# Kernel optimization log

Measured on AMD Instinct MI355X. Metric: run time of the kernel, lower is better.

Reference implementation:

```python
import jax, jax.numpy as jnp
import numpy as np
from jax import lax
from jax.scipy.special import logsumexp

GW_WEIGHT = 20.0
GAMMA_P = 0.01
IN_ITER = 5
OUT_ITER = 10
LAMBDA_STEP = 0.01
N1, N2, D = 2048, 2048, 128
EMB_SCALE = 0.05  # keeps exp(-x@x.T) numerically sane, mimics trained embeddings
ADJ_DENSITY = 0.005


def setup_inputs() -> dict:
    key = jax.random.key(0)
    k1, k2, k3, k4 = jax.random.split(key, 4)
    out1 = jax.random.normal(k1, (N1, D), jnp.float32) * EMB_SCALE
    out2 = jax.random.normal(k2, (N2, D), jnp.float32) * EMB_SCALE

    def make_adj(k, n):
        m = (jax.random.uniform(k, (n, n)) < ADJ_DENSITY).astype(jnp.float32)
        m = jnp.maximum(m, m.T)                      # symmetric, like to_dense_adj of undirected graph
        return m * (1.0 - jnp.eye(n, dtype=jnp.float32))

    adj1 = make_adj(k3, N1)
    adj2 = make_adj(k4, N2)
    threshold_lambda = jnp.float32(1.0 / (N1 * N2))  # init_lambda / (n1*n2)
    return {"out1": out1, "out2": out2, "adj1": adj1, "adj2": adj2,
            "threshold_lambda": threshold_lambda}


def sinkhorn_stable(inter_c, intra_c1, intra_c2, gw_weight, gamma_p, lam,
                    in_iter, out_iter):
    """Log-domain (stabilized) entropic GW Sinkhorn.
    Outer loop: linearize the GW cost around current plan s (shifted by lam);
    inner loop: stabilized Sinkhorn with uniform marginals."""
    n1, n2 = inter_c.shape
    dt = inter_c.dtype
    log_mu = jnp.full((n1,), -np.log(n1), dt)
    log_nu = jnp.full((n2,), -np.log(n2), dt)
    c1sq = intra_c1 ** 2
    c2sq = intra_c2 ** 2
    s0 = jnp.full((n1, n2), 1.0 / (n1 * n2), dt)

    def outer_body(_, s):
        s_hat = s - lam
        a = jnp.sum(s_hat, axis=1)                    # [n1]
        b = jnp.sum(s_hat, axis=0)                    # [n2]
        # GW cost linearization: c1^2 a 1^T + 1 b^T c2^2 - 2 c1 s c2^T
        gw_cost = ((c1sq @ a)[:, None] + (b @ c2sq)[None, :]
                   - 2.0 * (intra_c1 @ s_hat @ intra_c2.T))
        cost = inter_c + gw_weight * gw_cost
        K = -cost / gamma_p                           # log kernel

        def inner_body(_, uv):
            u, v = uv
            u = log_mu - logsumexp(K + v[None, :], axis=1)
            v = log_nu - logsumexp(K + u[:, None], axis=0)
            return (u, v)

        u, v = lax.fori_loop(0, in_iter, inner_body,
                             (jnp.zeros((n1,), dt), jnp.zeros((n2,), dt)))
        return jnp.exp(K + u[:, None] + v[None, :])

    return lax.fori_loop(0, out_iter, outer_body, s0)


def _update_lambda(inter_c, intra_c1, intra_c2, s, gw_weight):
    # mid = c1^2 @ 1 * n2 + 1 @ c2^2 * n1 - 2 c1 @ 1 @ c2^T is rank-structured;
    # compute sum(mid*s) and sum(mid) without materializing mid.
    n1, n2 = inter_c.shape
    c1sq = intra_c1 ** 2
    c2sq = intra_c2 ** 2
    r1sq = jnp.sum(c1sq, axis=1)      # rowsum of c1^2  [n1]
    c2s = jnp.sum(c2sq, axis=0)       # colsum of c2^2  [n2]
    rs1 = jnp.sum(intra_c1, axis=1)   # [n1]
    rs2 = jnp.sum(intra_c2, axis=1)   # [n2]
    a_s = jnp.sum(s, axis=1)
    b_s = jnp.sum(s, axis=0)
    k1 = jnp.sum(inter_c)
    k2 = n2 * (r1sq @ a_s) + n1 * (c2s @ b_s) - 2.0 * (rs1 @ (s @ rs2))
    k3 = (n2 * n2) * jnp.sum(r1sq) + (n1 * n1) * jnp.sum(c2s) \
         - 2.0 * jnp.sum(rs1) * jnp.sum(rs2)
    return (k1 + 2.0 * gw_weight * k2) / (2.0 * gw_weight * k3)


def reference(out1, out2, adj1, adj2, threshold_lambda):
    n1, n2 = out1.shape[0], out2.shape[0]
    inter_c = jnp.exp(-(out1 @ out2.T))
    intra_c1 = jnp.exp(-(out1 @ out1.T)) * adj1
    intra_c2 = jnp.exp(-(out2 @ out2.T)) * adj2

    # torch.no_grad() block
    s = sinkhorn_stable(inter_c, intra_c1, intra_c2, GW_WEIGHT, GAMMA_P,
                        threshold_lambda, IN_ITER, OUT_ITER)
    lam = (LAMBDA_STEP * _update_lambda(inter_c, intra_c1, intra_c2, s, GW_WEIGHT)
           + (1.0 - LAMBDA_STEP) * threshold_lambda)

    s_hat = s - lam
    w_loss = jnp.sum(inter_c * s_hat)
    a = jnp.sum(s_hat, axis=1)
    b = jnp.sum(s_hat, axis=0)
    c1sq = intra_c1 ** 2
    c2sq = intra_c2 ** 2
    gw_loss = jnp.sum(((c1sq @ a)[:, None] + (b @ c2sq)[None, :]
                       - 2.0 * (intra_c1 @ s_hat @ intra_c2.T)) * s_hat)
    loss = w_loss + GW_WEIGHT * gw_loss + 20.0
    return (loss, s, lam)
```

## Files before the change

kernel.cpp:

```cpp
#include <hip/hip_runtime.h>
#include <math.h>

#define N 2048
#define DIM 128
#define CAP (N*64)
#define LOGN 7.6246189861593985f

typedef unsigned long long u64;
typedef unsigned int u32;
typedef unsigned short u16;

__device__ __forceinline__ u32 bf16bits(float f) {
  u32 x = __float_as_uint(f);
  return (x + 0x7fffu + ((x >> 16) & 1u)) >> 16;
}
__device__ __forceinline__ u32 pack_bf16x2(float lo, float hi) {
  return bf16bits(lo) | (bf16bits(hi) << 16);
}
__device__ __forceinline__ float bflo(u32 u) { return __uint_as_float(u << 16); }
__device__ __forceinline__ float bfhi(u32 u) { return __uint_as_float(u & 0xffff0000u); }


__global__ __launch_bounds__(256) void k_gemm_inter(
    const float* __restrict__ A, const float* __restrict__ B,
    float* __restrict__ O, double* __restrict__ k1p) {
  __shared__ __align__(16) float As[64][65];
  __shared__ __align__(16) float Bs[64][65];
  __shared__ float red[256];
  const int t = threadIdx.x;
  const int i0 = blockIdx.y * 64, j0 = blockIdx.x * 64;
  const int tx = t & 15, ty = t >> 4;
  float acc[4][4] = {};
  for (int kk = 0; kk < DIM; kk += 64) {
    if (kk) __syncthreads();
    for (int q = t; q < 64 * 16; q += 256) {
      int row = q >> 4, k4 = (q & 15) << 2;
      float4 av = *(const float4*)&A[(size_t)(i0 + row) * DIM + kk + k4];
      As[k4 + 0][row] = av.x; As[k4 + 1][row] = av.y;
      As[k4 + 2][row] = av.z; As[k4 + 3][row] = av.w;
      float4 bv = *(const float4*)&B[(size_t)(j0 + row) * DIM + kk + k4];
      Bs[k4 + 0][row] = bv.x; Bs[k4 + 1][row] = bv.y;
      Bs[k4 + 2][row] = bv.z; Bs[k4 + 3][row] = bv.w;
    }
    __syncthreads();
    #pragma unroll 4
    for (int k = 0; k < 64; ++k) {
      float av[4], bv[4];
      #pragma unroll
      for (int d = 0; d < 4; ++d) { av[d] = As[k][ty * 4 + d]; bv[d] = Bs[k][tx * 4 + d]; }
      #pragma unroll
      for (int di = 0; di < 4; ++di)
        #pragma unroll
        for (int dj = 0; dj < 4; ++dj)
          acc[di][dj] = fmaf(av[di], bv[dj], acc[di][dj]);
    }
  }
  float psum = 0.f;
  #pragma unroll
  for (int di = 0; di < 4; ++di)
    #pragma unroll
    for (int dj = 0; dj < 4; ++dj) {
      float vv = __expf(-acc[di][dj]);
      O[(size_t)(i0 + ty * 4 + di) * N + (j0 + tx * 4 + dj)] = vv;
      psum += vv;
    }
  red[t] = psum; __syncthreads();
  for (int off = 128; off; off >>= 1) { if (t < off) red[t] += red[t + off]; __syncthreads(); }
  if (t == 0) k1p[blockIdx.y * 32 + blockIdx.x] = (double)red[0];
}

__global__ __launch_bounds__(256) void k_count(const float* __restrict__ adj, int* __restrict__ cnt) {
  int i = blockIdx.x * 4 + (threadIdx.x >> 6);
  int lane = threadIdx.x & 63;
  const float* row = adj + (size_t)i * N;
  int c = 0;
  for (int j = lane; j < N; j += 64) c += (row[j] != 0.f) ? 1 : 0;
  for (int off = 32; off; off >>= 1) c += __shfl_down(c, off);
  if (lane == 0) cnt[i] = c;
}

__global__ __launch_bounds__(256) void k_scan(const int* __restrict__ cnt, int* __restrict__ rp) {
  __shared__ int sums[256];
  int t = threadIdx.x;
  int local[8]; int run = 0;
  int base = t * 8;
  #pragma unroll
  for (int k = 0; k < 8; ++k) { local[k] = run; run += cnt[base + k]; }
  sums[t] = run; __syncthreads();
  for (int off = 1; off < 256; off <<= 1) {
    int val = (t >= off) ? sums[t - off] : 0;
    __syncthreads();
    sums[t] += val;
    __syncthreads();
  }
  int pre = (t == 0) ? 0 : sums[t - 1];
  #pragma unroll
  for (int k = 0; k < 8; ++k) rp[base + k] = pre + local[k];
  if (t == 255) rp[N] = sums[255];
}

__global__ __launch_bounds__(256) void k_fill(const float* __restrict__ adj, const int* __restrict__ rp,
                                              int* __restrict__ cols, int* __restrict__ rows) {
  int i = blockIdx.x * 4 + (threadIdx.x >> 6);
  int lane = threadIdx.x & 63;
  const float* row = adj + (size_t)i * N;
  int pos = rp[i];
  for (int j0 = 0; j0 < N; j0 += 64) {
    bool p = row[j0 + lane] != 0.f;
    u64 mask = __ballot(p);
    if (p) {
      int off = __popcll(mask & ((1ull << lane) - 1ull));
      cols[pos + off] = j0 + lane;
      rows[pos + off] = i;
    }
    pos += __popcll(mask);
  }
}

__global__ __launch_bounds__(256) void k_vals(const int* __restrict__ rp, const int* __restrict__ rows,
                                              const int* __restrict__ cols, float* __restrict__ vals,
                                              const float* __restrict__ emb) {
  int lane = threadIdx.x & 63;
  int total = rp[N];
  for (int p = blockIdx.x * 4 + (threadIdx.x >> 6); p < total; p += 8192) {
    int i = rows[p], k = cols[p];
    const float* ei = emb + (size_t)i * DIM;
    const float* ek = emb + (size_t)k * DIM;
    float s = ei[lane] * ek[lane] + ei[lane + 64] * ek[lane + 64];
    for (int off = 32; off; off >>= 1) s += __shfl_down(s, off);
    if (lane == 0) vals[p] = __expf(-s);
  }
}

__global__ __launch_bounds__(256) void k_rowstats(const int* __restrict__ rp, const float* __restrict__ vals,
                                                  float* __restrict__ rs, float* __restrict__ rsq) {
  int i = blockIdx.x * 4 + (threadIdx.x >> 6);
  int lane = threadIdx.x & 63;
  int p0 = rp[i], p1 = rp[i + 1];
  float s1 = 0.f, s2 = 0.f;
  for (int p = p0 + lane; p < p1; p += 64) { float w = vals[p]; s1 += w; s2 += w * w; }
  for (int off = 32; off; off >>= 1) { s1 += __shfl_down(s1, off); s2 += __shfl_down(s2, off); }
  if (lane == 0) { rs[i] = s1; rsq[i] = s2; }
}

template<int V>
__global__ __launch_bounds__(256) void k_spmmt(const int* __restrict__ rp, const int* __restrict__ cols,
                                               const float* __restrict__ vals, const u16* __restrict__ S,
                                               const float* __restrict__ af, const float* __restrict__ bf,
                                               u16* __restrict__ OutB, float* __restrict__ OutF) {
  __shared__ int winc[1024];
  __shared__ float winv[1024];
  __shared__ int rb[9];
  const int t = threadIdx.x;
  const int tile = blockIdx.x & 7;
  const int c = tile * 256 + t;
  const int i0 = (blockIdx.x >> 3) * 8;
  const int p0 = rp[i0];
  if (t < 9) rb[t] = rp[i0 + t] - p0;
  __syncthreads();
  const int nn = rb[8];
  for (int k = t; k < nn; k += 256) {
    int col = cols[p0 + k];
    winc[k] = col << 11;
    winv[k] = (V == 0) ? vals[p0 + k] * af[col] : vals[p0 + k];
  }
  __syncthreads();
  float a[8];
  #pragma unroll
  for (int r = 0; r < 8; ++r) {
    int pe = rb[r + 1];
    int p = rb[r];
    float a0 = 0.f, a1 = 0.f, a2 = 0.f, a3 = 0.f;
    for (; p + 3 < pe; p += 4) {
      a0 = fmaf(winv[p],     __uint_as_float((u32)S[winc[p]     + c] << 16), a0);
      a1 = fmaf(winv[p + 1], __uint_as_float((u32)S[winc[p + 1] + c] << 16), a1);
      a2 = fmaf(winv[p + 2], __uint_as_float((u32)S[winc[p + 2] + c] << 16), a2);
      a3 = fmaf(winv[p + 3], __uint_as_float((u32)S[winc[p + 3] + c] << 16), a3);
    }
    for (; p < pe; ++p) a0 = fmaf(winv[p], __uint_as_float((u32)S[winc[p] + c] << 16), a0);
    a[r] = (a0 + a1) + (a2 + a3);
  }
  size_t ob = (size_t)(tile * 256 + t) * N + i0;
  if (V == 0) {
    float bc = bf[c];
    #pragma unroll
    for (int r = 0; r < 8; ++r) a[r] *= bc;
    uint4 pk;
    pk.x = pack_bf16x2(a[0], a[1]); pk.y = pack_bf16x2(a[2], a[3]);
    pk.z = pack_bf16x2(a[4], a[5]); pk.w = pack_bf16x2(a[6], a[7]);
    *(uint4*)&OutB[ob] = pk;
  } else {
    *(float4*)&OutF[ob]     = make_float4(a[0], a[1], a[2], a[3]);
    *(float4*)&OutF[ob + 4] = make_float4(a[4], a[5], a[6], a[7]);
  }
}

__global__ __launch_bounds__(256) void k_prep(
    int mode,
    const int* __restrict__ rp1, const int* __restrict__ cols1, const float* __restrict__ vals1,
    const float* __restrict__ r1sq, const float* __restrict__ rs1,
    const float* __restrict__ r2sq, const float* __restrict__ lamp,
    const float* __restrict__ as_,
    float* __restrict__ Ai, float* __restrict__ Bj, float* __restrict__ RLi) {
  int g = blockIdx.x * 256 + threadIdx.x;
  float lam = *lamp;
  float f = 0.00048828125f - lam * 2048.f;
  if (mode == 0) {
    if (g < N) {
      Ai[g] = -2000.f * r1sq[g] * f;
      RLi[g] = 4000.f * rs1[g] * (2.384185791015625e-07f - lam);
    } else {
      int j = g - N;
      Bj[j] = -2000.f * r2sq[j] * f;
    }
  } else if (mode == 1) {
    if (g < N) {
      int p0 = rp1[g], p1 = rp1[g + 1];
      float acc = 0.f;
      for (int p = p0; p < p1; ++p) { float w = vals1[p]; acc = fmaf(w * w, as_[cols1[p]], acc); }
      Ai[g] = -2000.f * (acc - lam * 2048.f * r1sq[g]);
      RLi[g] = -4000.f * lam * rs1[g];
    } else {
      int j = g - N;
      Bj[j] = -2000.f * r2sq[j] * f;
    }
  } else {
    if (g < N) {
      int p0 = rp1[g], p1 = rp1[g + 1];
      float acc = 0.f;
      for (int p = p0; p < p1; ++p) { float w = vals1[p]; acc = fmaf(w * w, as_[cols1[p]], acc); }
      Ai[g] = acc;
    } else {
      int j = g - N;
      Bj[j] = r2sq[j] * 0.00048828125f;
    }
  }
}

template<int MODE>
__global__ __launch_bounds__(256) void k_iter(
    u32* __restrict__ P,
    const float* __restrict__ inter, const float* __restrict__ M,
    const float* __restrict__ Ai, const float* __restrict__ Bj,
    const float* __restrict__ RLi, const float* __restrict__ rs2,
    const float* __restrict__ bvec, float* __restrict__ avec,
    float* __restrict__ part) {
  __shared__ u32 Pl[4 * 1024];
  __shared__ float bl[N];
  __shared__ float a4[4];
  const int t = threadIdx.x;
  const int r0 = blockIdx.x * 4;
  const int w = t >> 6, lane = t & 63;
  const int row = r0 + w;

  if (MODE == 0) {
    #pragma unroll
    for (int q = 0; q < 2; ++q) {
      int j = (q * 256 + t) * 4;
      *(float4*)&bl[j] = *(const float4*)&bvec[j];
    }
    #pragma unroll
    for (int q = 0; q < 4; ++q) {
      int g = (q * 256 + t) * 4;
      *(uint4*)&Pl[g] = *(const uint4*)&P[(size_t)r0 * 1024 + g];
    }
    __syncthreads();
    float y = 0.f;
    const u32* Pr = Pl + w * 1024;
    #pragma unroll
    for (int k = 0; k < 16; ++k) {
      int g = lane + k * 64;
      u32 u = Pr[g];
      y = fmaf(bflo(u), bl[2 * g], y);
      y = fmaf(bfhi(u), bl[2 * g + 1], y);
    }
    for (int off = 32; off; off >>= 1) y += __shfl_xor(y, off);
    if (lane == 0) { float aw = 1.f / (2048.f * y); a4[w] = aw; avec[row] = aw; }
  } else {
    float kv[32];
    float m = -INFINITY;
    const float ai_ = Ai[row], rli = RLi[row];
    const float* ir = inter + (size_t)row * N;
    const float* mr = M + (size_t)row * N;
    #pragma unroll
    for (int q = 0; q < 8; ++q) {
      int j = lane * 4 + q * 256;
      float4 iv = *(const float4*)&ir[j];
      float4 bj = *(const float4*)&Bj[j];
      float4 r2 = *(const float4*)&rs2[j];
      float k0 = fmaf(-100.f, iv.x, ai_ + bj.x + rli * r2.x);
      float k1 = fmaf(-100.f, iv.y, ai_ + bj.y + rli * r2.y);
      float k2 = fmaf(-100.f, iv.z, ai_ + bj.z + rli * r2.z);
      float k3 = fmaf(-100.f, iv.w, ai_ + bj.w + rli * r2.w);
      if (MODE == 1) {
        float4 mv = *(const float4*)&mr[j];
        k0 = fmaf(4000.f, mv.x, k0);
        k1 = fmaf(4000.f, mv.y, k1);
        k2 = fmaf(4000.f, mv.z, k2);
        k3 = fmaf(4000.f, mv.w, k3);
      }
      kv[q * 4 + 0] = k0; kv[q * 4 + 1] = k1; kv[q * 4 + 2] = k2; kv[q * 4 + 3] = k3;
      m = fmaxf(m, fmaxf(fmaxf(k0, k1), fmaxf(k2, k3)));
    }
    for (int off = 32; off; off >>= 1) m = fmaxf(m, __shfl_xor(m, off));
    float ss = 0.f;
    #pragma unroll
    for (int q = 0; q < 8; ++q) {
      float p0 = __expf(kv[q * 4 + 0] - m);
      float p1 = __expf(kv[q * 4 + 1] - m);
      float p2 = __expf(kv[q * 4 + 2] - m);
      float p3 = __expf(kv[q * 4 + 3] - m);
      ss += (p0 + p1) + (p2 + p3);
      u32 lo = pack_bf16x2(p0, p1), hi = pack_bf16x2(p2, p3);
      int g = lane * 2 + q * 128;
      Pl[w * 1024 + g] = lo; Pl[w * 1024 + g + 1] = hi;
      *(uint2*)&P[(size_t)row * 1024 + g] = make_uint2(lo, hi);
    }
    for (int off = 32; off; off >>= 1) ss += __shfl_xor(ss, off);
    if (lane == 0) { float aw = 1.f / (2048.f * ss); a4[w] = aw; avec[row] = aw; }
  }
  __syncthreads();
  const float a0 = a4[0], a1 = a4[1], a2 = a4[2], a3 = a4[3];
  #pragma unroll
  for (int k = 0; k < 4; ++k) {
    int g = k * 256 + t;
    u32 u0 = Pl[g], u1 = Pl[1024 + g], u2 = Pl[2048 + g], u3 = Pl[3072 + g];
    float zlo = bflo(u0) * a0 + bflo(u1) * a1 + bflo(u2) * a2 + bflo(u3) * a3;
    float zhi = bfhi(u0) * a0 + bfhi(u1) * a1 + bfhi(u2) * a2 + bfhi(u3) * a3;
    *(float2*)&part[(size_t)blockIdx.x * N + 2 * g] = make_float2(zlo, zhi);
  }
}

__global__ __launch_bounds__(256) void k_comb(const float* __restrict__ part, float* __restrict__ bvec) {
  __shared__ float pp[16][17];
  const int t = threadIdx.x;
  const int cl = t & 15, kg = t >> 4;
  const int c = blockIdx.x * 16 + cl;
  float z = 0.f;
  for (int k = kg * 32; k < kg * 32 + 32; ++k) z += part[(size_t)k * N + c];
  pp[kg][cl] = z;
  __syncthreads();
  if (t < 16) {
    float zz = 0.f;
    #pragma unroll
    for (int g = 0; g < 16; ++g) zz += pp[g][t];
    bvec[blockIdx.x * 16 + t] = 1.f / (2048.f * zz);
  }
}

__global__ __launch_bounds__(256) void k_rowfin(const u32* __restrict__ P, const float* __restrict__ bvec,
                                                const float* __restrict__ avec, float* __restrict__ as_) {
  __shared__ float bl[N];
  const int t = threadIdx.x;
  #pragma unroll
  for (int q = 0; q < 2; ++q) {
    int j = (q * 256 + t) * 4;
    *(float4*)&bl[j] = *(const float4*)&bvec[j];
  }
  __syncthreads();
  const int w = t >> 6, lane = t & 63;
  const int row = blockIdx.x * 4 + w;
  const u32* Pr = P + (size_t)row * 1024;
  float y = 0.f;
  #pragma unroll
  for (int k = 0; k < 16; ++k) {
    int g = lane + k * 64;
    u32 u = Pr[g];
    y = fmaf(bflo(u), bl[2 * g], y);
    y = fmaf(bfhi(u), bl[2 * g + 1], y);
  }
  for (int off = 32; off; off >>= 1) y += __shfl_xor(y, off);
  if (lane == 0) as_[row] = avec[row] * y;
}

__global__ __launch_bounds__(256) void k_fstats(
    const float* __restrict__ inter, const u32* __restrict__ P, const float* __restrict__ M,
    const float* __restrict__ rs2, const float* __restrict__ avec, const float* __restrict__ bvec,
    float* __restrict__ sOut, float* __restrict__ sisr, float* __restrict__ yv,
    double* __restrict__ dotp) {
  __shared__ __align__(16) float r2[N];
  __shared__ __align__(16) float bl[N];
  __shared__ double redm[4];
  const int t = threadIdx.x;
  #pragma unroll
  for (int q = 0; q < 2; ++q) {
    int j = (q * 256 + t) * 4;
    *(float4*)&r2[j] = *(const float4*)&rs2[j];
    *(float4*)&bl[j] = *(const float4*)&bvec[j];
  }
  __syncthreads();
  const int w = t >> 6, lane = t & 63;
  const int row = blockIdx.x * 4 + w;
  const float av = avec[row];
  const float* ir = inter + (size_t)row * N;
  const float* mr = M + (size_t)row * N;
  const u32* Pr = P + (size_t)row * 1024;
  float* sr = sOut + (size_t)row * N;
  float d1 = 0.f, d2 = 0.f;
  double dm = 0.0;
  #pragma unroll 4
  for (int k = 0; k < 16; ++k) {
    int g = lane + k * 64;
    int j = 2 * g;
    u32 u = Pr[g];
    float s0 = bflo(u) * av * bl[j];
    float s1 = bfhi(u) * av * bl[j + 1];
    float2 iv = *(const float2*)&ir[j];
    float2 mv = *(const float2*)&mr[j];
    sr[j] = s0; sr[j + 1] = s1;
    d1 += iv.x * s0 + iv.y * s1;
    d2 += s0 * r2[j] + s1 * r2[j + 1];
    dm += (double)(mv.x * s0) + (double)(mv.y * s1);
  }
  for (int off = 32; off; off >>= 1) {
    d1 += __shfl_down(d1, off);
    d2 += __shfl_down(d2, off);
    dm += __shfl_down(dm, off);
  }
  if (lane == 0) { sisr[row] = d1; yv[row] = d2; redm[w] = dm; }
  __syncthreads();
  if (t == 0) dotp[blockIdx.x] = redm[0] + redm[1] + redm[2] + redm[3];
}

__global__ __launch_bounds__(256) void k_final(
    const float* __restrict__ paf, const float* __restrict__ pbf,
    const float* __restrict__ r1sq, const float* __restrict__ r2sq,
    const float* __restrict__ rs1, const float* __restrict__ rs2,
    const float* __restrict__ as_,
    const float* __restrict__ yv, const float* __restrict__ sisr,
    const double* __restrict__ k1p, const double* __restrict__ dotp,
    const float* __restrict__ lamp, float* __restrict__ out_loss, float* __restrict__ out_lam) {
  __shared__ double red[256];
  int t = threadIdx.x;
  auto dred = [&](double acc) -> double {
    red[t] = acc; __syncthreads();
    for (int off = 128; off; off >>= 1) { if (t < off) red[t] += red[t + off]; __syncthreads(); }
    double r = red[0]; __syncthreads();
    return r;
  };
  auto dotv = [&](const float* a, const float* b) -> double {
    double acc = 0.0;
    for (int k = t; k < N; k += 256) acc += (double)a[k] * (b ? (double)b[k] : 1.0);
    return dred(acc);
  };
  double k1a = 0.0;
  for (int k = t; k < 1024; k += 256) k1a += k1p[k];
  double k1 = dred(k1a);
  double sma = 0.0;
  for (int k = t; k < 512; k += 256) sma += dotp[k];
  double smfs = dred(sma);
  double paas = dotv(paf, as_);
  double pbbs = dotv(pbf, nullptr) * (1.0 / 2048.0);
  double r1as = dotv(r1sq, as_);
  double rs1y = dotv(rs1, yv);
  double sis  = dotv(sisr, nullptr);
  double sr1  = dotv(r1sq, nullptr);
  double sr2  = dotv(r2sq, nullptr);
  double ss1  = dotv(rs1, nullptr);
  double ss2  = dotv(rs2, nullptr);
  if (t == 0) {
    double c2bs = sr2 / 2048.0;
    double lam0 = (double)*lamp;
    double k2 = 2048.0 * r1as + 2048.0 * c2bs - 2.0 * rs1y;
    double k3 = 2048.0 * 2048.0 * (sr1 + sr2) - 2.0 * ss1 * ss2;
    double upd = (k1 + 40.0 * k2) / (40.0 * k3);
    double lamn = 0.01 * upd + 0.99 * lam0;
    double g1 = paas + pbbs - 2.0 * smfs;
    double wl = sis - lamn * k1;
    double gwl = g1 - 2.0 * lamn * k2 + lamn * lamn * k3;
    double loss = wl + 20.0 * gwl + 20.0;
    *out_loss = (float)loss;
    *out_lam = (float)lamn;
  }
}


extern "C" void kernel_launch(void* const* d_in, const int* in_sizes, int n_in,
                              void* d_out, int out_size, void* d_ws, size_t ws_size,
                              hipStream_t stream) {
  (void)in_sizes; (void)n_in; (void)out_size; (void)ws_size;
  const float* out1 = (const float*)d_in[0];
  const float* out2 = (const float*)d_in[1];
  const float* adj1 = (const float*)d_in[2];
  const float* adj2 = (const float*)d_in[3];
  const float* lamp = (const float*)d_in[4];
  float* o = (float*)d_out;
  float* sOut = o + 1;

  char* w = (char*)d_ws;
  size_t off = 0;
  auto alloc = [&](size_t bytes) -> void* {
    void* p = w + off;
    off = (off + bytes + 255) & ~(size_t)255;
    return p;
  };
  const size_t NNf = (size_t)N * N * sizeof(float);
  float* inter = (float*)alloc(NNf);
  float* Mbuf  = (float*)alloc(NNf);
  u32*  Pbuf   = (u32*)alloc((size_t)N * 1024 * sizeof(u32));
  u16*  Tth    = (u16*)alloc((size_t)N * N * sizeof(u16));
  int* rp1   = (int*)alloc((N + 1) * sizeof(int));
  int* rp2   = (int*)alloc((N + 1) * sizeof(int));
  int* cnt   = (int*)alloc(N * sizeof(int));
  int* cols1 = (int*)alloc(CAP * sizeof(int));
  int* rows1 = (int*)alloc(CAP * sizeof(int));
  int* cols2 = (int*)alloc(CAP * sizeof(int));
  int* rows2 = (int*)alloc(CAP * sizeof(int));
  float* vals1 = (float*)alloc(CAP * sizeof(float));
  float* vals2 = (float*)alloc(CAP * sizeof(float));
  float* r1sq = (float*)alloc(N * sizeof(float));
  float* rs1  = (float*)alloc(N * sizeof(float));
  float* r2sq = (float*)alloc(N * sizeof(float));
  float* rs2v = (float*)alloc(N * sizeof(float));
  float* asv  = (float*)alloc(N * sizeof(float));
  float* avec = (float*)alloc(N * sizeof(float));
  float* bvec = (float*)alloc(N * sizeof(float));
  float* Ai   = (float*)alloc(N * sizeof(float));
  float* Bj   = (float*)alloc(N * sizeof(float));
  float* RLi  = (float*)alloc(N * sizeof(float));
  float* yv   = (float*)alloc(N * sizeof(float));
  float* sisr = (float*)alloc(N * sizeof(float));
  float* part = (float*)alloc((size_t)512 * N * sizeof(float));
  double* k1p = (double*)alloc(1024 * sizeof(double));
  double* dotp= (double*)alloc(512 * sizeof(double));

  dim3 b(256);

  k_gemm_inter<<<dim3(32, 32), b, 0, stream>>>(out1, out2, inter, k1p);
  k_count<<<512, b, 0, stream>>>(adj1, cnt);
  k_scan<<<1, b, 0, stream>>>(cnt, rp1);
  k_count<<<512, b, 0, stream>>>(adj2, cnt);
  k_scan<<<1, b, 0, stream>>>(cnt, rp2);
  k_fill<<<512, b, 0, stream>>>(adj1, rp1, cols1, rows1);
  k_fill<<<512, b, 0, stream>>>(adj2, rp2, cols2, rows2);
  k_vals<<<2048, b, 0, stream>>>(rp1, rows1, cols1, vals1, out1);
  k_vals<<<2048, b, 0, stream>>>(rp2, rows2, cols2, vals2, out2);
  k_rowstats<<<512, b, 0, stream>>>(rp1, vals1, rs1, r1sq);
  k_rowstats<<<512, b, 0, stream>>>(rp2, vals2, rs2v, r2sq);

  for (int t = 0; t < 10; ++t) {
    k_prep<<<16, b, 0, stream>>>((t == 0) ? 0 : 1, rp1, cols1, vals1,
                                 r1sq, rs1, r2sq, lamp, asv, Ai, Bj, RLi);
    if (t > 0) {
      k_spmmt<0><<<2048, b, 0, stream>>>(rp1, cols1, vals1, (const u16*)Pbuf, avec, bvec, Tth, nullptr);
      k_spmmt<1><<<2048, b, 0, stream>>>(rp2, cols2, vals2, Tth, nullptr, nullptr, nullptr, Mbuf);
      k_iter<1><<<512, b, 0, stream>>>(Pbuf, inter, Mbuf, Ai, Bj, RLi, rs2v, bvec, avec, part);
    } else {
      k_iter<2><<<512, b, 0, stream>>>(Pbuf, inter, Mbuf, Ai, Bj, RLi, rs2v, bvec, avec, part);
    }
    k_comb<<<128, b, 0, stream>>>(part, bvec);
    for (int r = 1; r < 5; ++r) {
      k_iter<0><<<512, b, 0, stream>>>(Pbuf, inter, Mbuf, Ai, Bj, RLi, rs2v, bvec, avec, part);
      k_comb<<<128, b, 0, stream>>>(part, bvec);
    }
    k_rowfin<<<512, b, 0, stream>>>(Pbuf, bvec, avec, asv);
  }

  k_spmmt<0><<<2048, b, 0, stream>>>(rp1, cols1, vals1, (const u16*)Pbuf, avec, bvec, Tth, nullptr);
  k_spmmt<1><<<2048, b, 0, stream>>>(rp2, cols2, vals2, Tth, nullptr, nullptr, nullptr, Mbuf);
  k_prep<<<16, b, 0, stream>>>(2, rp1, cols1, vals1,
                               r1sq, rs1, r2sq, lamp, asv, Ai, Bj, RLi);
  k_fstats<<<512, b, 0, stream>>>(inter, Pbuf, Mbuf, rs2v, avec, bvec, sOut, sisr, yv, dotp);
  k_final<<<1, b, 0, stream>>>(Ai, Bj, r1sq, r2sq, rs1, rs2v, asv, yv, sisr,
                               k1p, dotp, lamp, o, o + 1 + (size_t)N * N);
}
```

Before: 1.201 ms.

## Store GW correction matrix in bf16, vectorize spmm reads, fold prep into iter

The second sparse-dense product now writes its N×N output as bf16 instead of fp32, and k_iter and k_fstats read it as packed bf16 pairs, halving that matrix's write and read traffic. k_spmmt now reads two bf16 columns per 32-bit load and handles 4 rows per block instead of 8. The per-outer-iteration k_prep launch is removed; its row terms are computed inside k_iter with a wave reduction, and the Bj vector is rebuilt from r2sq. This removes launches and bytes but lowers the precision of M, which is multiplied by 4000 inside the exponent.

```diff
diff --git a/kernel.cpp b/kernel.cpp
--- a/kernel.cpp
+++ b/kernel.cpp
@@ -145,104 +145,63 @@
 
 template<int V>
 __global__ __launch_bounds__(256) void k_spmmt(const int* __restrict__ rp, const int* __restrict__ cols,
-                                               const float* __restrict__ vals, const u16* __restrict__ S,
+                                               const float* __restrict__ vals, const u32* __restrict__ S,
                                                const float* __restrict__ af, const float* __restrict__ bf,
-                                               u16* __restrict__ OutB, float* __restrict__ OutF) {
-  __shared__ int winc[1024];
-  __shared__ float winv[1024];
-  __shared__ int rb[9];
+                                               u16* __restrict__ Out) {
+  __shared__ int winc[512];
+  __shared__ float winv[512];
+  __shared__ int rb[5];
   const int t = threadIdx.x;
-  const int tile = blockIdx.x & 7;
-  const int c = tile * 256 + t;
-  const int i0 = (blockIdx.x >> 3) * 8;
+  const int tile = blockIdx.x & 3;
+  const int cu = tile * 256 + t;
+  const int i0 = (blockIdx.x >> 2) * 4;
   const int p0 = rp[i0];
-  if (t < 9) rb[t] = rp[i0 + t] - p0;
-  __syncthreads();
-  const int nn = rb[8];
+  if (t < 5) rb[t] = rp[i0 + t] - p0;
+  __syncthreads();
+  const int nn = rb[4];
   for (int k = t; k < nn; k += 256) {
     int col = cols[p0 + k];
-    winc[k] = col << 11;
+    winc[k] = col << 10;
     winv[k] = (V == 0) ? vals[p0 + k] * af[col] : vals[p0 + k];
   }
   __syncthreads();
-  float a[8];
-  #pragma unroll
-  for (int r = 0; r < 8; ++r) {
-    int pe = rb[r + 1];
-    int p = rb[r];
-    float a0 = 0.f, a1 = 0.f, a2 = 0.f, a3 = 0.f;
-    for (; p + 3 < pe; p += 4) {
-      a0 = fmaf(winv[p],     __uint_as_float((u32)S[winc[p]     + c] << 16), a0);
-      a1 = fmaf(winv[p + 1], __uint_as_float((u32)S[winc[p + 1] + c] << 16), a1);
-      a2 = fmaf(winv[p + 2], __uint_as_float((u32)S[winc[p + 2] + c] << 16), a2);
-      a3 = fmaf(winv[p + 3], __uint_as_float((u32)S[winc[p + 3] + c] << 16), a3);
-    }
-    for (; p < pe; ++p) a0 = fmaf(winv[p], __uint_as_float((u32)S[winc[p] + c] << 16), a0);
-    a[r] = (a0 + a1) + (a2 + a3);
-  }
-  size_t ob = (size_t)(tile * 256 + t) * N + i0;
+  float alo[4], ahi[4];
+  #pragma unroll
+  for (int r = 0; r < 4; ++r) {
+    int pe = rb[r + 1], p = rb[r];
+    float l0 = 0.f, l1 = 0.f, h0 = 0.f, h1 = 0.f;
+    for (; p + 1 < pe; p += 2) {
+      u32 u0 = S[winc[p] + cu], u1 = S[winc[p + 1] + cu];
+      l0 = fmaf(winv[p],     bflo(u0), l0);  h0 = fmaf(winv[p],     bfhi(u0), h0);
+      l1 = fmaf(winv[p + 1], bflo(u1), l1);  h1 = fmaf(winv[p + 1], bfhi(u1), h1);
+    }
+    if (p < pe) {
+      u32 u = S[winc[p] + cu];
+      l0 = fmaf(winv[p], bflo(u), l0);  h0 = fmaf(winv[p], bfhi(u), h0);
+    }
+    alo[r] = l0 + l1; ahi[r] = h0 + h1;
+  }
+  const int c0 = cu * 2;
   if (V == 0) {
-    float bc = bf[c];
-    #pragma unroll
-    for (int r = 0; r < 8; ++r) a[r] *= bc;
-    uint4 pk;
-    pk.x = pack_bf16x2(a[0], a[1]); pk.y = pack_bf16x2(a[2], a[3]);
-    pk.z = pack_bf16x2(a[4], a[5]); pk.w = pack_bf16x2(a[6], a[7]);
-    *(uint4*)&OutB[ob] = pk;
-  } else {
-    *(float4*)&OutF[ob]     = make_float4(a[0], a[1], a[2], a[3]);
-    *(float4*)&OutF[ob + 4] = make_float4(a[4], a[5], a[6], a[7]);
-  }
-}
-
-__global__ __launch_bounds__(256) void k_prep(
-    int mode,
-    const int* __restrict__ rp1, const int* __restrict__ cols1, const float* __restrict__ vals1,
-    const float* __restrict__ r1sq, const float* __restrict__ rs1,
-    const float* __restrict__ r2sq, const float* __restrict__ lamp,
-    const float* __restrict__ as_,
-    float* __restrict__ Ai, float* __restrict__ Bj, float* __restrict__ RLi) {
-  int g = blockIdx.x * 256 + threadIdx.x;
-  float lam = *lamp;
-  float f = 0.00048828125f - lam * 2048.f;
-  if (mode == 0) {
-    if (g < N) {
-      Ai[g] = -2000.f * r1sq[g] * f;
-      RLi[g] = 4000.f * rs1[g] * (2.384185791015625e-07f - lam);
-    } else {
-      int j = g - N;
-      Bj[j] = -2000.f * r2sq[j] * f;
-    }
-  } else if (mode == 1) {
-    if (g < N) {
-      int p0 = rp1[g], p1 = rp1[g + 1];
-      float acc = 0.f;
-      for (int p = p0; p < p1; ++p) { float w = vals1[p]; acc = fmaf(w * w, as_[cols1[p]], acc); }
-      Ai[g] = -2000.f * (acc - lam * 2048.f * r1sq[g]);
-      RLi[g] = -4000.f * lam * rs1[g];
-    } else {
-      int j = g - N;
-      Bj[j] = -2000.f * r2sq[j] * f;
-    }
-  } else {
-    if (g < N) {
-      int p0 = rp1[g], p1 = rp1[g + 1];
-      float acc = 0.f;
-      for (int p = p0; p < p1; ++p) { float w = vals1[p]; acc = fmaf(w * w, as_[cols1[p]], acc); }
-      Ai[g] = acc;
-    } else {
-      int j = g - N;
-      Bj[j] = r2sq[j] * 0.00048828125f;
-    }
-  }
+    float2 bv = *(const float2*)&bf[c0];
+    #pragma unroll
+    for (int r = 0; r < 4; ++r) { alo[r] *= bv.x; ahi[r] *= bv.y; }
+  }
+  u32* O32 = (u32*)Out;
+  *(uint2*)&O32[(size_t)c0 * 1024 + (i0 >> 1)] =
+      make_uint2(pack_bf16x2(alo[0], alo[1]), pack_bf16x2(alo[2], alo[3]));
+  *(uint2*)&O32[(size_t)(c0 + 1) * 1024 + (i0 >> 1)] =
+      make_uint2(pack_bf16x2(ahi[0], ahi[1]), pack_bf16x2(ahi[2], ahi[3]));
 }
 
 template<int MODE>
 __global__ __launch_bounds__(256) void k_iter(
     u32* __restrict__ P,
-    const float* __restrict__ inter, const float* __restrict__ M,
-    const float* __restrict__ Ai, const float* __restrict__ Bj,
-    const float* __restrict__ RLi, const float* __restrict__ rs2,
+    const float* __restrict__ inter, const u32* __restrict__ M32,
+    const int* __restrict__ rp1, const int* __restrict__ cols1, const float* __restrict__ vals1,
+    const float* __restrict__ r1sq, const float* __restrict__ rs1,
+    const float* __restrict__ r2sq, const float* __restrict__ rs2,
+    const float* __restrict__ lamp, const float* __restrict__ asv_in,
     const float* __restrict__ bvec, float* __restrict__ avec,
     float* __restrict__ part) {
   __shared__ u32 Pl[4 * 1024];
@@ -277,27 +236,44 @@
     for (int off = 32; off; off >>= 1) y += __shfl_xor(y, off);
     if (lane == 0) { float aw = 1.f / (2048.f * y); a4[w] = aw; avec[row] = aw; }
   } else {
+    const float lam = *lamp;
+    const float f = 0.00048828125f - lam * 2048.f;
+    float ai_, rli;
+    if (MODE == 2) {
+      ai_ = -2000.f * r1sq[row] * f;
+      rli = 4000.f * rs1[row] * (2.384185791015625e-07f - lam);
+    } else {
+      int q0 = rp1[row], q1 = rp1[row + 1];
+      float acc = 0.f;
+      for (int p = q0 + lane; p < q1; p += 64) {
+        float wv = vals1[p];
+        acc = fmaf(wv * wv, asv_in[cols1[p]], acc);
+      }
+      for (int off = 32; off; off >>= 1) acc += __shfl_xor(acc, off);
+      ai_ = -2000.f * (acc - lam * 2048.f * r1sq[row]);
+      rli = -4000.f * lam * rs1[row];
+    }
+    const float bjf = -2000.f * f;
     float kv[32];
     float m = -INFINITY;
-    const float ai_ = Ai[row], rli = RLi[row];
     const float* ir = inter + (size_t)row * N;
-    const float* mr = M + (size_t)row * N;
+    const u32* mr = M32 + (size_t)row * 1024;
     #pragma unroll
     for (int q = 0; q < 8; ++q) {
       int j = lane * 4 + q * 256;
       float4 iv = *(const float4*)&ir[j];
-      float4 bj = *(const float4*)&Bj[j];
+      float4 rq = *(const float4*)&r2sq[j];
       float4 r2 = *(const float4*)&rs2[j];
-      float k0 = fmaf(-100.f, iv.x, ai_ + bj.x + rli * r2.x);
-      float k1 = fmaf(-100.f, iv.y, ai_ + bj.y + rli * r2.y);
-      float k2 = fmaf(-100.f, iv.z, ai_ + bj.z + rli * r2.z);
-      float k3 = fmaf(-100.f, iv.w, ai_ + bj.w + rli * r2.w);
+      float k0 = fmaf(-100.f, iv.x, fmaf(bjf, rq.x, ai_ + rli * r2.x));
+      float k1 = fmaf(-100.f, iv.y, fmaf(bjf, rq.y, ai_ + rli * r2.y));
+      float k2 = fmaf(-100.f, iv.z, fmaf(bjf, rq.z, ai_ + rli * r2.z));
+      float k3 = fmaf(-100.f, iv.w, fmaf(bjf, rq.w, ai_ + rli * r2.w));
       if (MODE == 1) {
-        float4 mv = *(const float4*)&mr[j];
-        k0 = fmaf(4000.f, mv.x, k0);
-        k1 = fmaf(4000.f, mv.y, k1);
-        k2 = fmaf(4000.f, mv.z, k2);
-        k3 = fmaf(4000.f, mv.w, k3);
+        uint2 mu = *(const uint2*)&mr[j >> 1];
+        k0 = fmaf(4000.f, bflo(mu.x), k0);
+        k1 = fmaf(4000.f, bfhi(mu.x), k1);
+        k2 = fmaf(4000.f, bflo(mu.y), k2);
+        k3 = fmaf(4000.f, bfhi(mu.y), k3);
       }
       kv[q * 4 + 0] = k0; kv[q * 4 + 1] = k1; kv[q * 4 + 2] = k2; kv[q * 4 + 3] = k3;
       m = fmaxf(m, fmaxf(fmaxf(k0, k1), fmaxf(k2, k3)));
@@ -373,8 +349,25 @@
   if (lane == 0) as_[row] = avec[row] * y;
 }
 
+
+__global__ __launch_bounds__(256) void k_prep2(
+    const int* __restrict__ rp1, const int* __restrict__ cols1, const float* __restrict__ vals1,
+    const float* __restrict__ r2sq, const float* __restrict__ as_,
+    float* __restrict__ paf, float* __restrict__ pbf) {
+  int g = blockIdx.x * 256 + threadIdx.x;
+  if (g < N) {
+    int p0 = rp1[g], p1 = rp1[g + 1];
+    float acc = 0.f;
+    for (int p = p0; p < p1; ++p) { float w = vals1[p]; acc = fmaf(w * w, as_[cols1[p]], acc); }
+    paf[g] = acc;
+  } else {
+    int j = g - N;
+    pbf[j] = r2sq[j] * 0.00048828125f;
+  }
+}
+
 __global__ __launch_bounds__(256) void k_fstats(
-    const float* __restrict__ inter, const u32* __restrict__ P, const float* __restrict__ M,
+    const float* __restrict__ inter, const u32* __restrict__ P, const u32* __restrict__ M32,
     const float* __restrict__ rs2, const float* __restrict__ avec, const float* __restrict__ bvec,
     float* __restrict__ sOut, float* __restrict__ sisr, float* __restrict__ yv,
     double* __restrict__ dotp) {
@@ -393,7 +386,7 @@
   const int row = blockIdx.x * 4 + w;
   const float av = avec[row];
   const float* ir = inter + (size_t)row * N;
-  const float* mr = M + (size_t)row * N;
+  const u32* mr = M32 + (size_t)row * 1024;
   const u32* Pr = P + (size_t)row * 1024;
   float* sr = sOut + (size_t)row * N;
   float d1 = 0.f, d2 = 0.f;
@@ -403,14 +396,14 @@
     int g = lane + k * 64;
     int j = 2 * g;
     u32 u = Pr[g];
+    u32 mu = mr[g];
     float s0 = bflo(u) * av * bl[j];
     float s1 = bfhi(u) * av * bl[j + 1];
     float2 iv = *(const float2*)&ir[j];
-    float2 mv = *(const float2*)&mr[j];
     sr[j] = s0; sr[j + 1] = s1;
     d1 += iv.x * s0 + iv.y * s1;
     d2 += s0 * r2[j] + s1 * r2[j + 1];
-    dm += (double)(mv.x * s0) + (double)(mv.y * s1);
+    dm += (double)(bflo(mu) * s0) + (double)(bfhi(mu) * s1);
   }
   for (int off = 32; off; off >>= 1) {
     d1 += __shfl_down(d1, off);
@@ -496,9 +489,9 @@
   };
   const size_t NNf = (size_t)N * N * sizeof(float);
   float* inter = (float*)alloc(NNf);
-  float* Mbuf  = (float*)alloc(NNf);
   u32*  Pbuf   = (u32*)alloc((size_t)N * 1024 * sizeof(u32));
   u16*  Tth    = (u16*)alloc((size_t)N * N * sizeof(u16));
+  u16*  Mb16   = (u16*)alloc((size_t)N * N * sizeof(u16));
   int* rp1   = (int*)alloc((N + 1) * sizeof(int));
   int* rp2   = (int*)alloc((N + 1) * sizeof(int));
   int* cnt   = (int*)alloc(N * sizeof(int));
@@ -515,11 +508,10 @@
   float* asv  = (float*)alloc(N * sizeof(float));
   float* avec = (float*)alloc(N * sizeof(float));
   float* bvec = (float*)alloc(N * sizeof(float));
-  float* Ai   = (float*)alloc(N * sizeof(float));
-  float* Bj   = (float*)alloc(N * sizeof(float));
-  float* RLi  = (float*)alloc(N * sizeof(float));
   float* yv   = (float*)alloc(N * sizeof(float));
   float* sisr = (float*)alloc(N * sizeof(float));
+  float* paf  = (float*)alloc(N * sizeof(float));
+  float* pbf  = (float*)alloc(N * sizeof(float));
   float* part = (float*)alloc((size_t)512 * N * sizeof(float));
   double* k1p = (double*)alloc(1024 * sizeof(double));
   double* dotp= (double*)alloc(512 * sizeof(double));
@@ -539,28 +531,28 @@
   k_rowstats<<<512, b, 0, stream>>>(rp2, vals2, rs2v, r2sq);
 
   for (int t = 0; t < 10; ++t) {
-    k_prep<<<16, b, 0, stream>>>((t == 0) ? 0 : 1, rp1, cols1, vals1,
-                                 r1sq, rs1, r2sq, lamp, asv, Ai, Bj, RLi);
     if (t > 0) {
-      k_spmmt<0><<<2048, b, 0, stream>>>(rp1, cols1, vals1, (const u16*)Pbuf, avec, bvec, Tth, nullptr);
-      k_spmmt<1><<<2048, b, 0, stream>>>(rp2, cols2, vals2, Tth, nullptr, nullptr, nullptr, Mbuf);
-      k_iter<1><<<512, b, 0, stream>>>(Pbuf, inter, Mbuf, Ai, Bj, RLi, rs2v, bvec, avec, part);
+      k_spmmt<0><<<2048, b, 0, stream>>>(rp1, cols1, vals1, Pbuf, avec, bvec, Tth);
+      k_spmmt<1><<<2048, b, 0, stream>>>(rp2, cols2, vals2, (const u32*)Tth, nullptr, nullptr, Mb16);
+      k_iter<1><<<512, b, 0, stream>>>(Pbuf, inter, (const u32*)Mb16, rp1, cols1, vals1,
+                                       r1sq, rs1, r2sq, rs2v, lamp, asv, bvec, avec, part);
     } else {
-      k_iter<2><<<512, b, 0, stream>>>(Pbuf, inter, Mbuf, Ai, Bj, RLi, rs2v, bvec, avec, part);
+      k_iter<2><<<512, b, 0, stream>>>(Pbuf, inter, (const u32*)Mb16, rp1, cols1, vals1,
+                                       r1sq, rs1, r2sq, rs2v, lamp, asv, bvec, avec, part);
     }
     k_comb<<<128, b, 0, stream>>>(part, bvec);
     for (int r = 1; r < 5; ++r) {
-      k_iter<0><<<512, b, 0, stream>>>(Pbuf, inter, Mbuf, Ai, Bj, RLi, rs2v, bvec, avec, part);
+      k_iter<0><<<512, b, 0, stream>>>(Pbuf, inter, (const u32*)Mb16, rp1, cols1, vals1,
+                                       r1sq, rs1, r2sq, rs2v, lamp, asv, bvec, avec, part);
       k_comb<<<128, b, 0, stream>>>(part, bvec);
     }
     k_rowfin<<<512, b, 0, stream>>>(Pbuf, bvec, avec, asv);
   }
 
-  k_spmmt<0><<<2048, b, 0, stream>>>(rp1, cols1, vals1, (const u16*)Pbuf, avec, bvec, Tth, nullptr);
-  k_spmmt<1><<<2048, b, 0, stream>>>(rp2, cols2, vals2, Tth, nullptr, nullptr, nullptr, Mbuf);
-  k_prep<<<16, b, 0, stream>>>(2, rp1, cols1, vals1,
-                               r1sq, rs1, r2sq, lamp, asv, Ai, Bj, RLi);
-  k_fstats<<<512, b, 0, stream>>>(inter, Pbuf, Mbuf, rs2v, avec, bvec, sOut, sisr, yv, dotp);
-  k_final<<<1, b, 0, stream>>>(Ai, Bj, r1sq, r2sq, rs1, rs2v, asv, yv, sisr,
+  k_spmmt<0><<<2048, b, 0, stream>>>(rp1, cols1, vals1, Pbuf, avec, bvec, Tth);
+  k_spmmt<1><<<2048, b, 0, stream>>>(rp2, cols2, vals2, (const u32*)Tth, nullptr, nullptr, Mb16);
+  k_prep2<<<16, b, 0, stream>>>(rp1, cols1, vals1, r2sq, asv, paf, pbf);
+  k_fstats<<<512, b, 0, stream>>>(inter, Pbuf, (const u32*)Mb16, rs2v, avec, bvec, sOut, sisr, yv, dotp);
+  k_final<<<1, b, 0, stream>>>(paf, pbf, r1sq, r2sq, rs1, rs2v, asv, yv, sisr,
                                k1p, dotp, lamp, o, o + 1 + (size_t)N * N);
 }
```

After: 1.037 ms. 1.16x faster.
